# Kernel tuning notes

Measured on AMD Instinct MI355X. Metric: run time of the kernel, lower is better.

The kernel has to match this reference:

```python
import jax, jax.numpy as jnp
import numpy as np

N_NODES = 50000
N_EDGES = 800000
D_FEAT = 128
UNITS = 256
K = 3


def setup_inputs() -> dict:
    key = jax.random.key(0)
    k1, k2, k3, k4 = jax.random.split(key, 4)
    x = jax.random.normal(k1, (N_NODES, D_FEAT), dtype=jnp.float32)
    edge_index = jax.random.randint(k2, (2, N_EDGES), 0, N_NODES, dtype=jnp.int32)
    edge_weight = jnp.ones((N_EDGES,), dtype=jnp.float32)
    # glorot-uniform kernel [(K+1)*D, UNITS], zero bias
    fan_in, fan_out = D_FEAT * (K + 1), UNITS
    limit = np.sqrt(6.0 / (fan_in + fan_out)).astype(np.float32)
    kernel = jax.random.uniform(k3, (fan_in, fan_out), minval=-limit, maxval=limit, dtype=jnp.float32)
    bias = jnp.zeros((UNITS,), dtype=jnp.float32)
    return {"x": x, "edge_index": edge_index, "edge_weight": edge_weight,
            "kernel": kernel, "bias": bias}


def reference(x, edge_index, edge_weight, kernel, bias):
    n = x.shape[0]
    row, col = edge_index[0], edge_index[1]
    # symmetric GCN normalization (renorm=False: normalize first, then self-loops w=1)
    deg = jax.ops.segment_sum(edge_weight, row, num_segments=n)
    deg_inv_sqrt = jnp.where(deg > 0, jax.lax.rsqrt(jnp.where(deg > 0, deg, 1.0)), 0.0)
    normed_w = deg_inv_sqrt[row] * edge_weight * deg_inv_sqrt[col]
    loop = jnp.arange(n, dtype=row.dtype)
    row2 = jnp.concatenate([row, loop])
    col2 = jnp.concatenate([col, loop])
    w2 = jnp.concatenate([normed_w, jnp.ones((n,), dtype=normed_w.dtype)])
    # K-hop propagation, collecting each hop
    xs = [x]
    h = x
    for _ in range(K):
        msg = h[col2] * w2[:, None]            # [E+N, D] gather + scale
        h = jax.ops.segment_sum(msg, row2, num_segments=n)  # scatter-sum
        xs.append(h)
    hcat = jnp.concatenate(xs, axis=-1)        # [N, (K+1)*D]
    out = hcat @ kernel + bias
    return jax.nn.relu(out)
```

## Files before the change

### kernel.cpp

```cpp
#include <hip/hip_runtime.h>

#define NN 50000
#define NP 50048
#define NE 800000
#define D 128
#define UNITS 256
#define KTOT 512
#define SCAN_NB 50
#define NREP 8

typedef __attribute__((ext_vector_type(8))) short short8;
typedef __attribute__((ext_vector_type(4))) float floatx4;

__device__ inline unsigned short f2b(float f) {
    unsigned u = __float_as_uint(f);
    return (unsigned short)((u + 0x7fff + ((u >> 16) & 1)) >> 16);
}
__device__ inline float2 bx2f(unsigned v) {
    float2 r;
    r.x = __uint_as_float(v << 16);
    r.y = __uint_as_float(v & 0xffff0000u);
    return r;
}

__global__ void count_kernel(const int* __restrict__ row, int* __restrict__ cnt8,
                             int* __restrict__ rank, int E) {
    int e = blockIdx.x * blockDim.x + threadIdx.x;
    if (e < E) {
        int rep = (e >> 6) & (NREP - 1);
        rank[e] = atomicAdd(&cnt8[rep * NN + row[e]], 1);
    }
}

__global__ __launch_bounds__(256) void scanA_kernel(int* __restrict__ cnt8,
                                                    int* __restrict__ row_ptr,
                                                    int* __restrict__ bsum) {
    __shared__ int s[256];
    int b = blockIdx.x, t = threadIdx.x;
    int base = b * 1024 + t * 4;
    int v[4];
    int sum = 0;
#pragma unroll
    for (int i = 0; i < 4; ++i) {
        int idx = base + i;
        int tot = 0;
        if (idx < NN) {
            int c[NREP];
            int run = 0;
#pragma unroll
            for (int r = 0; r < NREP; ++r) c[r] = cnt8[r * NN + idx];
#pragma unroll
            for (int r = 0; r < NREP; ++r) {
                cnt8[r * NN + idx] = run;
                run += c[r];
            }
            tot = run;
        }
        v[i] = tot;
        sum += tot;
    }
    s[t] = sum;
    __syncthreads();
    for (int off = 1; off < 256; off <<= 1) {
        int add = (t >= off) ? s[t - off] : 0;
        __syncthreads();
        s[t] += add;
        __syncthreads();
    }
    int run = s[t] - sum;
#pragma unroll
    for (int i = 0; i < 4; ++i) {
        int idx = base + i;
        if (idx < NN) row_ptr[idx] = run;
        run += v[i];
    }
    if (t == 255) bsum[b] = s[255];
}

__global__ void scanB_kernel(int* __restrict__ bsum, int* __restrict__ row_ptr) {
    if (threadIdx.x == 0 && blockIdx.x == 0) {
        int run = 0;
        for (int i = 0; i < SCAN_NB; ++i) {
            int v = bsum[i];
            bsum[i] = run;
            run += v;
        }
        row_ptr[NN] = run;
    }
}

__global__ __launch_bounds__(256) void scanC_kernel(int* __restrict__ row_ptr,
                                                    const int* __restrict__ bsum) {
    int b = blockIdx.x, t = threadIdx.x;
    int off = bsum[b];
    int base = b * 1024 + t * 4;
#pragma unroll
    for (int i = 0; i < 4; ++i) {
        int idx = base + i;
        if (idx < NN) row_ptr[idx] += off;
    }
}

__global__ void fill_kernel(const int* __restrict__ row, const int* __restrict__ col,
                            const float* __restrict__ w, const int* __restrict__ rank,
                            const int* __restrict__ row_ptr, const int* __restrict__ cnt8,
                            int2* __restrict__ edges, int E) {
    int e = blockIdx.x * blockDim.x + threadIdx.x;
    if (e >= E) return;
    int r = row[e];
    int rep = (e >> 6) & (NREP - 1);
    int pos = row_ptr[r] + cnt8[rep * NN + r] + rank[e];
    edges[pos] = make_int2(col[e], __float_as_int(w[e]));
}

__global__ __launch_bounds__(256) void degdis_kernel(const int* __restrict__ row_ptr,
                                                     const int2* __restrict__ edges,
                                                     float* __restrict__ dis) {
    int node = blockIdx.x * 4 + (threadIdx.x >> 6);
    int l = threadIdx.x & 63;
    if (node >= NN) return;
    int beg = row_ptr[node], end = row_ptr[node + 1];
    float s = 0.f;
    for (int e = beg + l; e < end; e += 64) s += __int_as_float(edges[e].y);
#pragma unroll
    for (int off = 32; off; off >>= 1) s += __shfl_down(s, off);
    if (l == 0) dis[node] = s > 0.f ? rsqrtf(s) : 0.f;
}

__global__ __launch_bounds__(256) void norm_kernel(const int* __restrict__ row_ptr,
                                                   const float* __restrict__ dis,
                                                   int2* __restrict__ edges) {
    int node = blockIdx.x * 4 + (threadIdx.x >> 6);
    int l = threadIdx.x & 63;
    if (node >= NN) return;
    int beg = row_ptr[node], end = row_ptr[node + 1];
    float dr = dis[node];
    for (int e = beg + l; e < end; e += 64) {
        int2 E = edges[e];
        edges[e].y = __float_as_int(dr * __int_as_float(E.y) * dis[E.x]);
    }
}

__global__ void convx_kernel(const float* __restrict__ x, unsigned* __restrict__ xb) {
    int t = blockIdx.x * blockDim.x + threadIdx.x;
    float4 v = ((const float4*)x)[t];
    uint2 o;
    o.x = (unsigned)f2b(v.x) | ((unsigned)f2b(v.y) << 16);
    o.y = (unsigned)f2b(v.z) | ((unsigned)f2b(v.w) << 16);
    ((uint2*)xb)[t] = o;
}

__global__ __launch_bounds__(256) void transw_kernel(const float* __restrict__ W,
                                                     short* __restrict__ Wt) {
    __shared__ float tile[32][33];
    int kb = blockIdx.x * 32;
    int nb = blockIdx.y * 32;
    int tx = threadIdx.x & 31, ty = threadIdx.x >> 5;
    for (int i = 0; i < 32; i += 8)
        tile[ty + i][tx] = W[(size_t)(kb + ty + i) * UNITS + nb + tx];
    __syncthreads();
    for (int i = 0; i < 32; i += 8)
        Wt[(size_t)(nb + ty + i) * KTOT + kb + tx] = (short)f2b(tile[tx][ty + i]);
}

__device__ inline void acc8(float* acc, uint4 v, float w) {
    float2 f0 = bx2f(v.x), f1 = bx2f(v.y), f2 = bx2f(v.z), f3 = bx2f(v.w);
    acc[0] = fmaf(w, f0.x, acc[0]); acc[1] = fmaf(w, f0.y, acc[1]);
    acc[2] = fmaf(w, f1.x, acc[2]); acc[3] = fmaf(w, f1.y, acc[3]);
    acc[4] = fmaf(w, f2.x, acc[4]); acc[5] = fmaf(w, f2.y, acc[5]);
    acc[6] = fmaf(w, f3.x, acc[6]); acc[7] = fmaf(w, f3.y, acc[7]);
}

__global__ __launch_bounds__(256) void gather_kernel(const unsigned* __restrict__ hprev,
                                                     unsigned* __restrict__ hnext,
                                                     const int* __restrict__ row_ptr,
                                                     const int2* __restrict__ edges) {
    int node = blockIdx.x * 4 + (threadIdx.x >> 6);
    if (node >= NN) return;
    int l = threadIdx.x & 63;
    int g = l >> 4;
    int s = l & 15;
    const uint4* hp4 = (const uint4*)hprev;
    int beg = row_ptr[node], end = row_ptr[node + 1];

    float acc[8] = {0.f, 0.f, 0.f, 0.f, 0.f, 0.f, 0.f, 0.f};
    for (int e = beg; e < end; e += 8) {
        int i0 = e + g;
        int i1 = e + 4 + g;
        int2 E0 = edges[i0 < end ? i0 : end - 1];
        int2 E1 = edges[i1 < end ? i1 : end - 1];
        float w0 = (i0 < end) ? __int_as_float(E0.y) : 0.f;
        float w1 = (i1 < end) ? __int_as_float(E1.y) : 0.f;
        uint4 v0 = hp4[(size_t)E0.x * 16 + s];
        uint4 v1 = hp4[(size_t)E1.x * 16 + s];
        acc8(acc, v0, w0);
        acc8(acc, v1, w1);
    }
#pragma unroll
    for (int i = 0; i < 8; ++i) {
        acc[i] += __shfl_xor(acc[i], 16);
        acc[i] += __shfl_xor(acc[i], 32);
    }
    if (g == 0) {
        uint4 sv = hp4[(size_t)node * 16 + s];
        acc8(acc, sv, 1.f);
        uint4 o;
        o.x = (unsigned)f2b(acc[0]) | ((unsigned)f2b(acc[1]) << 16);
        o.y = (unsigned)f2b(acc[2]) | ((unsigned)f2b(acc[3]) << 16);
        o.z = (unsigned)f2b(acc[4]) | ((unsigned)f2b(acc[5]) << 16);
        o.w = (unsigned)f2b(acc[6]) | ((unsigned)f2b(acc[7]) << 16);
        ((uint4*)hnext)[(size_t)node * 16 + s] = o;
    }
}

#define BK 64
#define GLDS(g, l)                                                                      \
    __builtin_amdgcn_global_load_lds((const __attribute__((address_space(1))) void*)(g), \
                                     (__attribute__((address_space(3))) void*)(l), 16, 0, 0)

__global__ __launch_bounds__(256) void gemm_mfma(const short* __restrict__ A0,
                                                 const short* __restrict__ Wt,
                                                 const float* __restrict__ bias,
                                                 float* __restrict__ C) {
    __shared__ short As[128 * BK];
    __shared__ short Bs[128 * BK];
    const int t = threadIdx.x;
    const int m0 = blockIdx.x * 128;
    const int n0 = blockIdx.y * 128;
    const int w = t >> 6;
    const int l = t & 63;
    const int wr = (w >> 1) * 64;
    const int wc = (w & 1) * 64;
    const int lm = l & 15;
    const int lg = l >> 4;

    const int srow = l >> 3;
    const int soff = ((l & 7) ^ srow) * 8;

    floatx4 zero = {0.f, 0.f, 0.f, 0.f};
    floatx4 acc[4][4];
#pragma unroll
    for (int r = 0; r < 4; ++r)
#pragma unroll
        for (int c = 0; c < 4; ++c) acc[r][c] = zero;

    for (int kk = 0; kk < KTOT; kk += BK) {
        const short* Asrc = A0 + (size_t)(kk >> 7) * ((size_t)NP * 128) + (kk & 127);
        const short* Bsrc = Wt + kk;
#pragma unroll
        for (int i = 0; i < 4; ++i) {
            int seg = w * 4 + i;
            int row = seg * 8 + srow;
            GLDS(Asrc + (size_t)(m0 + row) * D + soff, As + seg * 512);
            GLDS(Bsrc + (size_t)(n0 + row) * KTOT + soff, Bs + seg * 512);
        }
        __syncthreads();
#pragma unroll
        for (int j = 0; j < 2; ++j) {
            short8 af[4], bfr[4];
#pragma unroll
            for (int r = 0; r < 4; ++r) {
                int row = wr + r * 16 + lm;
                int ch = (lg + 4 * j) ^ (row & 7);
                af[r] = *(const short8*)&As[row * BK + ch * 8];
            }
#pragma unroll
            for (int c = 0; c < 4; ++c) {
                int row = wc + c * 16 + lm;
                int ch = (lg + 4 * j) ^ (row & 7);
                bfr[c] = *(const short8*)&Bs[row * BK + ch * 8];
            }
#pragma unroll
            for (int r = 0; r < 4; ++r)
#pragma unroll
                for (int c = 0; c < 4; ++c)
                    acc[r][c] = __builtin_amdgcn_mfma_f32_16x16x32_bf16(af[r], bfr[c],
                                                                        acc[r][c], 0, 0, 0);
        }
        __syncthreads();
    }

    const int q4 = lg * 4;
#pragma unroll
    for (int r = 0; r < 4; ++r) {
#pragma unroll
        for (int i = 0; i < 4; ++i) {
            int m = m0 + wr + r * 16 + q4 + i;
            if (m < NN) {
#pragma unroll
                for (int c = 0; c < 4; ++c) {
                    int n = n0 + wc + c * 16 + lm;
                    float v = acc[r][c][i] + bias[n];
                    C[(size_t)m * UNITS + n] = fmaxf(v, 0.f);
                }
            }
        }
    }
}

extern "C" void kernel_launch(void* const* d_in, const int* in_sizes, int n_in,
                              void* d_out, int out_size, void* d_ws, size_t ws_size,
                              hipStream_t stream) {
    const float* x = (const float*)d_in[0];
    const int* ei = (const int*)d_in[1];
    const float* ew_in = (const float*)d_in[2];
    const float* W = (const float*)d_in[3];
    const float* bias = (const float*)d_in[4];
    float* out = (float*)d_out;

    const int* row = ei;
    const int* col = ei + NE;

    float* dis = (float*)d_ws;
    int* cnt8 = (int*)(dis + NN);
    int* rank = cnt8 + NREP * NN;
    int* bsum = rank + NE;
    int* row_ptr = bsum + 64;
    int2* edges = (int2*)(row_ptr + NN + 2);
    unsigned* xb = (unsigned*)(edges + NE) + 2;
    unsigned* h1b = xb + (size_t)NP * 64;
    unsigned* h2b = h1b + (size_t)NP * 64;
    unsigned* h3b = h2b + (size_t)NP * 64;
    short* Wt = (short*)(h3b + (size_t)NP * 64);

    hipMemsetAsync(cnt8, 0, NREP * NN * sizeof(int), stream);

    count_kernel<<<(NE + 255) / 256, 256, 0, stream>>>(row, cnt8, rank, NE);
    scanA_kernel<<<SCAN_NB, 256, 0, stream>>>(cnt8, row_ptr, bsum);
    scanB_kernel<<<1, 64, 0, stream>>>(bsum, row_ptr);
    scanC_kernel<<<SCAN_NB, 256, 0, stream>>>(row_ptr, bsum);
    fill_kernel<<<(NE + 255) / 256, 256, 0, stream>>>(row, col, ew_in, rank, row_ptr, cnt8,
                                                      edges, NE);
    degdis_kernel<<<(NN + 3) / 4, 256, 0, stream>>>(row_ptr, edges, dis);
    norm_kernel<<<(NN + 3) / 4, 256, 0, stream>>>(row_ptr, dis, edges);

    convx_kernel<<<(NN * D / 4) / 256, 256, 0, stream>>>(x, xb);
    transw_kernel<<<dim3(KTOT / 32, UNITS / 32), 256, 0, stream>>>(W, Wt);

    int gat_blocks = (NN + 3) / 4;
    gather_kernel<<<gat_blocks, 256, 0, stream>>>(xb, h1b, row_ptr, edges);
    gather_kernel<<<gat_blocks, 256, 0, stream>>>(h1b, h2b, row_ptr, edges);
    gather_kernel<<<gat_blocks, 256, 0, stream>>>(h2b, h3b, row_ptr, edges);

    gemm_mfma<<<dim3(NP / 128, UNITS / 128), 256, 0, stream>>>(
        (const short*)xb, Wt, bias, out);
}
```

Before: 318.5 us.

## Fuse edge normalization into first gather and merge prep kernels

```diff
diff --git a/kernel.cpp b/kernel.cpp
--- a/kernel.cpp
+++ b/kernel.cpp
@@ -7,7 +7,8 @@
 #define UNITS 256
 #define KTOT 512
 #define SCAN_NB 50
-#define NREP 8
+#define NREP 16
+#define CONV_NB 6250
 
 typedef __attribute__((ext_vector_type(8))) short short8;
 typedef __attribute__((ext_vector_type(4))) float floatx4;
@@ -23,16 +24,16 @@
     return r;
 }
 
-__global__ void count_kernel(const int* __restrict__ row, int* __restrict__ cnt8,
+__global__ void count_kernel(const int* __restrict__ row, int* __restrict__ cnt16,
                              int* __restrict__ rank, int E) {
     int e = blockIdx.x * blockDim.x + threadIdx.x;
     if (e < E) {
         int rep = (e >> 6) & (NREP - 1);
-        rank[e] = atomicAdd(&cnt8[rep * NN + row[e]], 1);
-    }
-}
-
-__global__ __launch_bounds__(256) void scanA_kernel(int* __restrict__ cnt8,
+        rank[e] = atomicAdd(&cnt16[rep * NN + row[e]], 1);
+    }
+}
+
+__global__ __launch_bounds__(256) void scanA_kernel(int* __restrict__ cnt16,
                                                     int* __restrict__ row_ptr,
                                                     int* __restrict__ bsum) {
     __shared__ int s[256];
@@ -48,10 +49,10 @@
             int c[NREP];
             int run = 0;
 #pragma unroll
-            for (int r = 0; r < NREP; ++r) c[r] = cnt8[r * NN + idx];
+            for (int r = 0; r < NREP; ++r) c[r] = cnt16[r * NN + idx];
 #pragma unroll
             for (int r = 0; r < NREP; ++r) {
-                cnt8[r * NN + idx] = run;
+                cnt16[r * NN + idx] = run;
                 run += c[r];
             }
             tot = run;
@@ -103,13 +104,13 @@
 
 __global__ void fill_kernel(const int* __restrict__ row, const int* __restrict__ col,
                             const float* __restrict__ w, const int* __restrict__ rank,
-                            const int* __restrict__ row_ptr, const int* __restrict__ cnt8,
+                            const int* __restrict__ row_ptr, const int* __restrict__ cnt16,
                             int2* __restrict__ edges, int E) {
     int e = blockIdx.x * blockDim.x + threadIdx.x;
     if (e >= E) return;
     int r = row[e];
     int rep = (e >> 6) & (NREP - 1);
-    int pos = row_ptr[r] + cnt8[rep * NN + r] + rank[e];
+    int pos = row_ptr[r] + cnt16[rep * NN + r] + rank[e];
     edges[pos] = make_int2(col[e], __float_as_int(w[e]));
 }
 
@@ -127,40 +128,29 @@
     if (l == 0) dis[node] = s > 0.f ? rsqrtf(s) : 0.f;
 }
 
-__global__ __launch_bounds__(256) void norm_kernel(const int* __restrict__ row_ptr,
-                                                   const float* __restrict__ dis,
-                                                   int2* __restrict__ edges) {
-    int node = blockIdx.x * 4 + (threadIdx.x >> 6);
-    int l = threadIdx.x & 63;
-    if (node >= NN) return;
-    int beg = row_ptr[node], end = row_ptr[node + 1];
-    float dr = dis[node];
-    for (int e = beg + l; e < end; e += 64) {
-        int2 E = edges[e];
-        edges[e].y = __float_as_int(dr * __int_as_float(E.y) * dis[E.x]);
-    }
-}
-
-__global__ void convx_kernel(const float* __restrict__ x, unsigned* __restrict__ xb) {
-    int t = blockIdx.x * blockDim.x + threadIdx.x;
-    float4 v = ((const float4*)x)[t];
-    uint2 o;
-    o.x = (unsigned)f2b(v.x) | ((unsigned)f2b(v.y) << 16);
-    o.y = (unsigned)f2b(v.z) | ((unsigned)f2b(v.w) << 16);
-    ((uint2*)xb)[t] = o;
-}
-
-__global__ __launch_bounds__(256) void transw_kernel(const float* __restrict__ W,
-                                                     short* __restrict__ Wt) {
+__global__ __launch_bounds__(256) void prep_kernel(const float* __restrict__ x,
+                                                   unsigned* __restrict__ xb,
+                                                   const float* __restrict__ W,
+                                                   short* __restrict__ Wt) {
     __shared__ float tile[32][33];
-    int kb = blockIdx.x * 32;
-    int nb = blockIdx.y * 32;
-    int tx = threadIdx.x & 31, ty = threadIdx.x >> 5;
-    for (int i = 0; i < 32; i += 8)
-        tile[ty + i][tx] = W[(size_t)(kb + ty + i) * UNITS + nb + tx];
-    __syncthreads();
-    for (int i = 0; i < 32; i += 8)
-        Wt[(size_t)(nb + ty + i) * KTOT + kb + tx] = (short)f2b(tile[tx][ty + i]);
+    if (blockIdx.x < CONV_NB) {
+        int t = blockIdx.x * 256 + threadIdx.x;
+        float4 v = ((const float4*)x)[t];
+        uint2 o;
+        o.x = (unsigned)f2b(v.x) | ((unsigned)f2b(v.y) << 16);
+        o.y = (unsigned)f2b(v.z) | ((unsigned)f2b(v.w) << 16);
+        ((uint2*)xb)[t] = o;
+    } else {
+        int b = blockIdx.x - CONV_NB;
+        int kb = (b & 15) * 32;
+        int nb = (b >> 4) * 32;
+        int tx = threadIdx.x & 31, ty = threadIdx.x >> 5;
+        for (int i = 0; i < 32; i += 8)
+            tile[ty + i][tx] = W[(size_t)(kb + ty + i) * UNITS + nb + tx];
+        __syncthreads();
+        for (int i = 0; i < 32; i += 8)
+            Wt[(size_t)(nb + ty + i) * KTOT + kb + tx] = (short)f2b(tile[tx][ty + i]);
+    }
 }
 
 __device__ inline void acc8(float* acc, uint4 v, float w) {
@@ -171,10 +161,12 @@
     acc[6] = fmaf(w, f3.x, acc[6]); acc[7] = fmaf(w, f3.y, acc[7]);
 }
 
+template <bool NORM>
 __global__ __launch_bounds__(256) void gather_kernel(const unsigned* __restrict__ hprev,
                                                      unsigned* __restrict__ hnext,
                                                      const int* __restrict__ row_ptr,
-                                                     const int2* __restrict__ edges) {
+                                                     int2* __restrict__ edges,
+                                                     const float* __restrict__ dis) {
     int node = blockIdx.x * 4 + (threadIdx.x >> 6);
     if (node >= NN) return;
     int l = threadIdx.x & 63;
@@ -182,19 +174,33 @@
     int s = l & 15;
     const uint4* hp4 = (const uint4*)hprev;
     int beg = row_ptr[node], end = row_ptr[node + 1];
+    float dr = NORM ? dis[node] : 1.f;
 
     float acc[8] = {0.f, 0.f, 0.f, 0.f, 0.f, 0.f, 0.f, 0.f};
     for (int e = beg; e < end; e += 8) {
         int i0 = e + g;
         int i1 = e + 4 + g;
-        int2 E0 = edges[i0 < end ? i0 : end - 1];
-        int2 E1 = edges[i1 < end ? i1 : end - 1];
-        float w0 = (i0 < end) ? __int_as_float(E0.y) : 0.f;
-        float w1 = (i1 < end) ? __int_as_float(E1.y) : 0.f;
-        uint4 v0 = hp4[(size_t)E0.x * 16 + s];
-        uint4 v1 = hp4[(size_t)E1.x * 16 + s];
+        long long p0 = __builtin_nontemporal_load(
+            (const long long*)&edges[i0 < end ? i0 : end - 1]);
+        long long p1 = __builtin_nontemporal_load(
+            (const long long*)&edges[i1 < end ? i1 : end - 1]);
+        int c0 = (int)p0, c1 = (int)p1;
+        float w0 = __int_as_float((int)(p0 >> 32));
+        float w1 = __int_as_float((int)(p1 >> 32));
+        if (NORM) {
+            w0 *= dr * dis[c0];
+            w1 *= dr * dis[c1];
+        }
+        w0 = (i0 < end) ? w0 : 0.f;
+        w1 = (i1 < end) ? w1 : 0.f;
+        uint4 v0 = hp4[(size_t)c0 * 16 + s];
+        uint4 v1 = hp4[(size_t)c1 * 16 + s];
         acc8(acc, v0, w0);
         acc8(acc, v1, w1);
+        if (NORM && s == 0) {
+            if (i0 < end) edges[i0].y = __float_as_int(w0);
+            if (i1 < end) edges[i1].y = __float_as_int(w1);
+        }
     }
 #pragma unroll
     for (int i = 0; i < 8; ++i) {
@@ -312,8 +318,8 @@
     const int* col = ei + NE;
 
     float* dis = (float*)d_ws;
-    int* cnt8 = (int*)(dis + NN);
-    int* rank = cnt8 + NREP * NN;
+    int* cnt16 = (int*)(dis + NN);
+    int* rank = cnt16 + NREP * NN;
     int* bsum = rank + NE;
     int* row_ptr = bsum + 64;
     int2* edges = (int2*)(row_ptr + NN + 2);
@@ -323,24 +329,21 @@
     unsigned* h3b = h2b + (size_t)NP * 64;
     short* Wt = (short*)(h3b + (size_t)NP * 64);
 
-    hipMemsetAsync(cnt8, 0, NREP * NN * sizeof(int), stream);
-
-    count_kernel<<<(NE + 255) / 256, 256, 0, stream>>>(row, cnt8, rank, NE);
-    scanA_kernel<<<SCAN_NB, 256, 0, stream>>>(cnt8, row_ptr, bsum);
+    hipMemsetAsync(cnt16, 0, NREP * NN * sizeof(int), stream);
+
+    count_kernel<<<(NE + 255) / 256, 256, 0, stream>>>(row, cnt16, rank, NE);
+    scanA_kernel<<<SCAN_NB, 256, 0, stream>>>(cnt16, row_ptr, bsum);
     scanB_kernel<<<1, 64, 0, stream>>>(bsum, row_ptr);
     scanC_kernel<<<SCAN_NB, 256, 0, stream>>>(row_ptr, bsum);
-    fill_kernel<<<(NE + 255) / 256, 256, 0, stream>>>(row, col, ew_in, rank, row_ptr, cnt8,
+    fill_kernel<<<(NE + 255) / 256, 256, 0, stream>>>(row, col, ew_in, rank, row_ptr, cnt16,
                                                       edges, NE);
     degdis_kernel<<<(NN + 3) / 4, 256, 0, stream>>>(row_ptr, edges, dis);
-    norm_kernel<<<(NN + 3) / 4, 256, 0, stream>>>(row_ptr, dis, edges);
-
-    convx_kernel<<<(NN * D / 4) / 256, 256, 0, stream>>>(x, xb);
-    transw_kernel<<<dim3(KTOT / 32, UNITS / 32), 256, 0, stream>>>(W, Wt);
+    prep_kernel<<<CONV_NB + 128, 256, 0, stream>>>(x, xb, W, Wt);
 
     int gat_blocks = (NN + 3) / 4;
-    gather_kernel<<<gat_blocks, 256, 0, stream>>>(xb, h1b, row_ptr, edges);
-    gather_kernel<<<gat_blocks, 256, 0, stream>>>(h1b, h2b, row_ptr, edges);
-    gather_kernel<<<gat_blocks, 256, 0, stream>>>(h2b, h3b, row_ptr, edges);
+    gather_kernel<true><<<gat_blocks, 256, 0, stream>>>(xb, h1b, row_ptr, edges, dis);
+    gather_kernel<false><<<gat_blocks, 256, 0, stream>>>(h1b, h2b, row_ptr, edges, dis);
+    gather_kernel<false><<<gat_blocks, 256, 0, stream>>>(h2b, h3b, row_ptr, edges, dis);
 
     gemm_mfma<<<dim3(NP / 128, UNITS / 128), 256, 0, stream>>>(
         (const short*)xb, Wt, bias, out);
```

Measured after the change: 325.6 us. +2.2%, slower.
